# Kernel optimization log

Hardware: AMD Instinct MI355X
Metric: run time of the kernel (lower is better)

The kernel has to match this reference:

```python
import jax, jax.numpy as jnp
import numpy as np

B, V, E = 8, 12288, 98304   # batch, nodes (healpix nside=32), edges (~8 nbrs/node)
FIN, FOUT, K = 256, 256, 4  # channels, Chebyshev order
EPS = 1e-5                  # BatchNorm1d eps


def setup_inputs() -> dict:
    key = jax.random.key(0)
    ks = jax.random.split(key, 5)
    x = jax.random.normal(ks[0], (B, V, FIN), jnp.float32)
    edge_src = jax.random.randint(ks[1], (E,), 0, V, dtype=jnp.int32)
    edge_dst = jax.random.randint(ks[2], (E,), 0, V, dtype=jnp.int32)
    edge_weight = jax.random.normal(ks[3], (E,), jnp.float32) * 0.3
    scale = (2.0 / (FIN * K)) ** 0.5  # kaiming-style init over K*Fin fan-in
    weight = jax.random.normal(ks[4], (K, FIN, FOUT), jnp.float32) * scale
    bias = jnp.zeros((FOUT,), jnp.float32)
    gamma = jnp.ones((FOUT,), jnp.float32)
    beta = jnp.zeros((FOUT,), jnp.float32)
    return {"x": x, "edge_weight": edge_weight, "weight": weight, "bias": bias,
            "gamma": gamma, "beta": beta, "edge_src": edge_src, "edge_dst": edge_dst}


def reference(x, edge_weight, weight, bias, gamma, beta, edge_src, edge_dst):
    # --- ConvCheb: Chebyshev polynomial recursion over sparse Laplacian ---
    xt = x.transpose(1, 0, 2)  # [V, B, Fin] (node-major for segment scatter)

    def lmul(y):  # sparse L @ y, y: [V, B, Fin]
        msg = edge_weight[:, None, None] * y[edge_src]          # [E, B, Fin]
        return jax.ops.segment_sum(msg, edge_dst, num_segments=V)

    xs = [xt]                                  # T_0(L) x = x
    if K > 1:
        xs.append(lmul(xt))                    # T_1(L) x = L x
    for _ in range(2, K):
        xs.append(2.0 * lmul(xs[-1]) - xs[-2])  # T_k = 2 L T_{k-1} - T_{k-2}
    xk = jnp.stack(xs)                         # [K, V, B, Fin]

    out = jnp.einsum('kvbi,kio->bvo', xk, weight) + bias  # [B, V, Fout]

    # --- BatchNorm1d over channels (training-mode batch stats over B,V) ---
    mean = out.mean(axis=(0, 1))
    var = out.var(axis=(0, 1))  # biased variance, as torch uses for normalization
    out = gamma * (out - mean) * jax.lax.rsqrt(var + EPS) + beta

    return jax.nn.relu(out)
```

## Files before the change

### kernel.cpp

```cpp
#include <hip/hip_runtime.h>

#define Vn    12288
#define En    98304
#define Mrows 98304

typedef unsigned short u16;
typedef u16   u16x8  __attribute__((ext_vector_type(8)));
typedef __bf16 bf16x8 __attribute__((ext_vector_type(8)));
typedef float f32x4  __attribute__((ext_vector_type(4)));

struct __align__(8) Edge { int s; float w; };

__device__ __forceinline__ float bf2f(u16 u) {
    union { float f; unsigned int i; } c; c.i = ((unsigned int)u) << 16; return c.f;
}
__device__ __forceinline__ u16 f2bf(float f) {
    union { float f; unsigned int i; } c; c.f = f;
    unsigned int r = c.i + 0x7fffu + ((c.i >> 16) & 1u);
    return (u16)(r >> 16);
}
__device__ __forceinline__ void load_lds16(const void* g, void* l) {
    __builtin_amdgcn_global_load_lds(
        (const __attribute__((address_space(1))) void*)g,
        (__attribute__((address_space(3))) void*)l, 16, 0, 0);
}

__global__ void cvt_k(const float* __restrict__ x, u16* __restrict__ xb) {
    int v = blockIdx.x;
    int t = threadIdx.x;
    int b = t >> 5, i = (t & 31) * 8;
    const float* p = x + ((size_t)b * Vn + v) * 256 + i;
    f32x4 a0 = *(const f32x4*)p;
    f32x4 a1 = *(const f32x4*)(p + 4);
    u16x8 r;
    #pragma unroll
    for (int j = 0; j < 4; ++j) { r[j] = f2bf(a0[j]); r[4 + j] = f2bf(a1[j]); }
    *(u16x8*)(xb + (size_t)v * 2048 + b * 256 + i) = r;
}

__global__ void wtrans_k(const float* __restrict__ w, u16* __restrict__ wt) {
    int kk = blockIdx.x;
    int o  = threadIdx.x;
    wt[(size_t)o * 1024 + kk] = f2bf(w[(size_t)kk * 256 + o]);
}

__global__ void count_k(const int* __restrict__ dst, int* __restrict__ counts) {
    int e = blockIdx.x * 256 + threadIdx.x;
    atomicAdd(&counts[dst[e]], 1);
}

__global__ void scan_k(const int* __restrict__ counts, int* __restrict__ row_start,
                       int* __restrict__ cursor) {
    __shared__ int par[1024];
    int t = threadIdx.x;
    int base = t * 12;
    int s = 0;
    #pragma unroll
    for (int i = 0; i < 12; ++i) s += counts[base + i];
    par[t] = s;
    __syncthreads();
    for (int off = 1; off < 1024; off <<= 1) {
        int v_ = (t >= off) ? par[t - off] : 0;
        __syncthreads();
        par[t] += v_;
        __syncthreads();
    }
    int run = (t == 0) ? 0 : par[t - 1];
    for (int i = 0; i < 12; ++i) {
        row_start[base + i] = run;
        cursor[base + i]    = run;
        run += counts[base + i];
    }
    if (t == 1023) row_start[Vn] = En;
}

__global__ void fill_k(const int* __restrict__ src, const int* __restrict__ dst,
                       const float* __restrict__ ew, int* __restrict__ cursor,
                       Edge* __restrict__ csr) {
    int e = blockIdx.x * 256 + threadIdx.x;
    int d = dst[e];
    int p = atomicAdd(&cursor[d], 1);
    Edge ed; ed.s = src[e]; ed.w = ew[e];
    csr[p] = ed;
}

template<int PREV>
__global__ __launch_bounds__(256)
void lmul_k(const u16* __restrict__ yb, const u16* __restrict__ prevb,
            u16* __restrict__ outb, const int* __restrict__ row_start,
            const Edge* __restrict__ csr)
{
    int slice = blockIdx.x & 7;
    int v     = (blockIdx.x >> 3) * 8 + (threadIdx.x >> 5);
    int t     = threadIdx.x & 31;
    int s0    = row_start[v];
    int cnt   = row_start[v + 1] - s0;
    size_t soff = (size_t)slice * 256 + (size_t)t * 8;
    float acc[8] = {0.f,0.f,0.f,0.f,0.f,0.f,0.f,0.f};
    for (int j0 = 0; j0 < cnt; j0 += 8) {
        int ss[8]; float ww[8];
        #pragma unroll
        for (int u = 0; u < 8; ++u) {
            int j = j0 + u;
            bool ok = j < cnt;
            Edge e = csr[s0 + (ok ? j : 0)];
            ss[u] = e.s; ww[u] = ok ? e.w : 0.f;
        }
        u16x8 g[8];
        #pragma unroll
        for (int u = 0; u < 8; ++u)
            g[u] = *(const u16x8*)(yb + (size_t)ss[u] * 2048 + soff);
        #pragma unroll
        for (int u = 0; u < 8; ++u)
            #pragma unroll
            for (int j8 = 0; j8 < 8; ++j8) acc[j8] += ww[u] * bf2f(g[u][j8]);
    }
    u16x8 r;
    if (PREV) {
        u16x8 pu = *(const u16x8*)(prevb + (size_t)v * 2048 + soff);
        #pragma unroll
        for (int j8 = 0; j8 < 8; ++j8) r[j8] = f2bf(2.0f * acc[j8] - bf2f(pu[j8]));
    } else {
        #pragma unroll
        for (int j8 = 0; j8 < 8; ++j8) r[j8] = f2bf(acc[j8]);
    }
    *(u16x8*)(outb + (size_t)v * 2048 + soff) = r;
}

__device__ __forceinline__ void stage_tile(const u16* __restrict__ Ak, int k0,
                                           const u16* __restrict__ wt, int kt,
                                           int m0, int tid, int wave,
                                           char* bufA, char* bufB)
{
    #pragma unroll
    for (int r = 0; r < 2; ++r) {
        int g  = r * 512 + tid;
        int ml = g >> 3;
        int c  = (g & 7) ^ (ml & 7);
        load_lds16(Ak + ((size_t)(m0 + ml)) * 256 + k0 + c * 8,
                   bufA + r * 8192 + wave * 1024);
    }
    #pragma unroll
    for (int r = 0; r < 4; ++r) {
        int g = r * 512 + tid;
        int o = g >> 3;
        int c = (g & 7) ^ (o & 7);
        load_lds16(wt + (size_t)o * 1024 + kt * 64 + c * 8,
                   bufB + r * 8192 + wave * 1024);
    }
}

__global__ __launch_bounds__(512)
void gemm_k(const u16* __restrict__ x0, const u16* __restrict__ x1,
            const u16* __restrict__ x2, const u16* __restrict__ x3,
            const u16* __restrict__ wt, const float* __restrict__ bias,
            u16* cbp, float* __restrict__ sums, float* __restrict__ sumsq)
{
    alignas(16) __shared__ char lds[147456];
    int tid  = threadIdx.x;
    int wave = tid >> 6;
    int lane = tid & 63;
    int m0   = blockIdx.x * 128;
    int wm   = wave & 1;
    int wn   = wave >> 1;

    f32x4 acc[4][4];
    #pragma unroll
    for (int a = 0; a < 4; ++a)
        #pragma unroll
        for (int b = 0; b < 4; ++b) acc[a][b] = (f32x4){0.f,0.f,0.f,0.f};

    stage_tile(x0, 0,  wt, 0, m0, tid, wave, (char*)lds,         (char*)lds + 16384);
    stage_tile(x0, 64, wt, 1, m0, tid, wave, (char*)lds + 49152, (char*)lds + 49152 + 16384);

    int cb = 0;
    int pb = 2;
    for (int t = 0; t < 16; ++t) {
        if (t < 15) asm volatile("s_waitcnt vmcnt(6) lgkmcnt(0)" ::: "memory");
        else        asm volatile("s_waitcnt vmcnt(0) lgkmcnt(0)" ::: "memory");
        __builtin_amdgcn_s_barrier();
        __builtin_amdgcn_sched_barrier(0);
        if (t < 14) {
            int kt = t + 2;
            int ks = kt >> 2;
            int k0 = (kt & 3) * 64;
            const u16* Ak = (ks == 0) ? x0 : (ks == 1) ? x1 : (ks == 2) ? x2 : x3;
            stage_tile(Ak, k0, wt, kt, m0, tid, wave,
                       (char*)lds + pb * 49152, (char*)lds + pb * 49152 + 16384);
        }
        const char* Ab = (const char*)lds + cb * 49152;
        const char* Bb = Ab + 16384;
        #pragma unroll
        for (int kstep = 0; kstep < 2; ++kstep) {
            int cidx = kstep * 4 + (lane >> 4);
            int row  = lane & 15;
            bf16x8 af[4], bfr[4];
            #pragma unroll
            for (int mt = 0; mt < 4; ++mt) {
                int m16 = wm * 64 + mt * 16 + row;
                af[mt] = *(const bf16x8*)(Ab + (size_t)(m16 * 8 + (cidx ^ (m16 & 7))) * 16);
            }
            #pragma unroll
            for (int nt = 0; nt < 4; ++nt) {
                int ol = wn * 64 + nt * 16 + row;
                bfr[nt] = *(const bf16x8*)(Bb + (size_t)(ol * 8 + (cidx ^ (ol & 7))) * 16);
            }
            __builtin_amdgcn_s_setprio(1);
            #pragma unroll
            for (int mt = 0; mt < 4; ++mt)
                #pragma unroll
                for (int nt = 0; nt < 4; ++nt)
                    acc[mt][nt] = __builtin_amdgcn_mfma_f32_16x16x32_bf16(
                        af[mt], bfr[nt], acc[mt][nt], 0, 0, 0);
            __builtin_amdgcn_s_setprio(0);
        }
        cb = (cb == 2) ? 0 : cb + 1;
        pb = (pb == 2) ? 0 : pb + 1;
    }

    __syncthreads();
    int crow = lane & 15, quad = lane >> 4;
    #pragma unroll
    for (int nt = 0; nt < 4; ++nt) {
        int o = wn * 64 + nt * 16 + crow;
        int c_o = o >> 3, o_in = (o & 7) * 2;
        float bv = bias[o];
        float ps = 0.f, pq = 0.f;
        #pragma unroll
        for (int mt = 0; mt < 4; ++mt) {
            #pragma unroll
            for (int r = 0; r < 4; ++r) {
                int ml = wm * 64 + mt * 16 + quad * 4 + r;
                u16 q = f2bf(acc[mt][nt][r] + bv);
                float vq = bf2f(q);
                *(u16*)(lds + (size_t)ml * 512 + (size_t)(c_o ^ (ml & 7)) * 16 + o_in) = q;
                ps += vq; pq += vq * vq;
            }
        }
        ps += __shfl_down(ps, 32, 64);  pq += __shfl_down(pq, 32, 64);
        ps += __shfl_down(ps, 16, 64);  pq += __shfl_down(pq, 16, 64);
        if (quad == 0) { atomicAdd(&sums[o], ps); atomicAdd(&sumsq[o], pq); }
    }
    __syncthreads();
    #pragma unroll
    for (int rr = 0; rr < 8; ++rr) {
        int ch = rr * 512 + tid;
        int ml = ch >> 5, c = ch & 31;
        u16x8 vv = *(const u16x8*)(lds + (size_t)ml * 512 + (size_t)(c ^ (ml & 7)) * 16);
        *(u16x8*)(cbp + (size_t)(m0 + ml) * 256 + c * 8) = vv;
    }
}

__global__ void finalize_k(const float* __restrict__ sums, const float* __restrict__ sumsq,
                           const float* __restrict__ gamma, const float* __restrict__ beta,
                           float* __restrict__ scale, float* __restrict__ shift) {
    int o = threadIdx.x;
    const float invM = 1.0f / (float)Mrows;
    float mean = sums[o] * invM;
    float var  = sumsq[o] * invM - mean * mean;
    float sc   = gamma[o] * rsqrtf(var + 1e-5f);
    scale[o] = sc;
    shift[o] = beta[o] - mean * sc;
}

__global__ void bn_relu_k(const u16* __restrict__ cb, float* __restrict__ outp,
                          const float* __restrict__ scale, const float* __restrict__ shift) {
    __shared__ float ssc[256], ssh[256];
    int t = threadIdx.x;
    ssc[t] = scale[t]; ssh[t] = shift[t];
    __syncthreads();
    size_t p = ((size_t)blockIdx.x * 256 + t) * 8;
    int o0 = (int)(p & 255);
    int m  = (int)(p >> 8);
    u16x8 v = *(const u16x8*)(cb + p);
    float* dst = outp + ((size_t)((m & 7) * Vn + (m >> 3))) * 256 + o0;
    f32x4 a, c;
    #pragma unroll
    for (int i = 0; i < 4; ++i) {
        a[i] = fmaxf(bf2f(v[i])     * ssc[o0 + i]     + ssh[o0 + i],     0.f);
        c[i] = fmaxf(bf2f(v[4 + i]) * ssc[o0 + 4 + i] + ssh[o0 + 4 + i], 0.f);
    }
    __builtin_nontemporal_store(a, (f32x4*)dst);
    __builtin_nontemporal_store(c, (f32x4*)(dst + 4));
}

extern "C" void kernel_launch(void* const* d_in, const int* in_sizes, int n_in,
                              void* d_out, int out_size, void* d_ws, size_t ws_size,
                              hipStream_t stream) {
    const float* x     = (const float*)d_in[0];
    const float* ew    = (const float*)d_in[1];
    const float* w     = (const float*)d_in[2];
    const float* bias  = (const float*)d_in[3];
    const float* gamma = (const float*)d_in[4];
    const float* beta  = (const float*)d_in[5];
    const int*   esrc  = (const int*)d_in[6];
    const int*   edst  = (const int*)d_in[7];
    float* outp = (float*)d_out;
    char*  ws   = (char*)d_ws;

    u16*   xb        = (u16*)  (ws + 0);
    u16*   x1        = (u16*)  (ws + 50331648);
    u16*   x2        = (u16*)  (ws + 100663296);
    u16*   x3        = (u16*)  (ws + 150994944);
    u16*   wt        = (u16*)  (ws + 201326592);
    Edge*  csr       = (Edge*) (ws + 201850880);
    int*   counts    = (int*)  (ws + 202637312);
    int*   row_start = (int*)  (ws + 202686464);
    int*   cursor    = (int*)  (ws + 202736128);
    float* sums      = (float*)(ws + 202785280);
    float* sumsq     = (float*)(ws + 202786304);
    float* scale     = (float*)(ws + 202787328);
    float* shift     = (float*)(ws + 202788352);

    hipMemsetAsync(counts, 0, 49152, stream);
    hipMemsetAsync(sums, 0, 2048, stream);

    cvt_k<<<Vn, 256, 0, stream>>>(x, xb);
    wtrans_k<<<1024, 256, 0, stream>>>(w, wt);
    count_k<<<384, 256, 0, stream>>>(edst, counts);
    scan_k<<<1, 1024, 0, stream>>>(counts, row_start, cursor);
    fill_k<<<384, 256, 0, stream>>>(esrc, edst, ew, cursor, csr);

    lmul_k<0><<<Vn, 256, 0, stream>>>(xb, nullptr, x1, row_start, csr);
    lmul_k<1><<<Vn, 256, 0, stream>>>(x1, xb,      x2, row_start, csr);
    lmul_k<1><<<Vn, 256, 0, stream>>>(x2, x1,      x3, row_start, csr);

    gemm_k<<<Mrows / 128, 512, 0, stream>>>(xb, x1, x2, x3, wt, bias,
                                            (u16*)x1, sums, sumsq);

    finalize_k<<<1, 256, 0, stream>>>(sums, sumsq, gamma, beta, scale, shift);
    bn_relu_k<<<12288, 256, 0, stream>>>((const u16*)x1, outp, scale, shift);
}
```

Before: 467.7 us.

## Tile weight transpose via LDS, fold BN finalize into apply kernel, nontemporal loads

```diff
diff --git a/kernel.cpp b/kernel.cpp
--- a/kernel.cpp
+++ b/kernel.cpp
@@ -30,8 +30,8 @@
     int t = threadIdx.x;
     int b = t >> 5, i = (t & 31) * 8;
     const float* p = x + ((size_t)b * Vn + v) * 256 + i;
-    f32x4 a0 = *(const f32x4*)p;
-    f32x4 a1 = *(const f32x4*)(p + 4);
+    f32x4 a0 = __builtin_nontemporal_load((const f32x4*)p);
+    f32x4 a1 = __builtin_nontemporal_load((const f32x4*)(p + 4));
     u16x8 r;
     #pragma unroll
     for (int j = 0; j < 4; ++j) { r[j] = f2bf(a0[j]); r[4 + j] = f2bf(a1[j]); }
@@ -39,9 +39,22 @@
 }
 
 __global__ void wtrans_k(const float* __restrict__ w, u16* __restrict__ wt) {
-    int kk = blockIdx.x;
-    int o  = threadIdx.x;
-    wt[(size_t)o * 1024 + kk] = f2bf(w[(size_t)kk * 256 + o]);
+    __shared__ u16 tile[32][1026];
+    int o0 = blockIdx.x * 32;
+    int t  = threadIdx.x;
+    int lo = t & 31;
+    int kr = t >> 5;
+    for (int kk0 = 0; kk0 < 1024; kk0 += 8) {
+        int kk = kk0 + kr;
+        tile[lo][kk] = f2bf(w[(size_t)kk * 256 + o0 + lo]);
+    }
+    __syncthreads();
+    for (int i = 0; i < 16; ++i) {
+        int ch = i * 256 + t;
+        int r = ch >> 7, c = ch & 127;
+        u16x8 vv = *(const u16x8*)(&tile[r][c * 8]);
+        *(u16x8*)(wt + (size_t)(o0 + r) * 1024 + c * 8) = vv;
+    }
 }
 
 __global__ void count_k(const int* __restrict__ dst, int* __restrict__ counts) {
@@ -251,28 +264,24 @@
     }
 }
 
-__global__ void finalize_k(const float* __restrict__ sums, const float* __restrict__ sumsq,
-                           const float* __restrict__ gamma, const float* __restrict__ beta,
-                           float* __restrict__ scale, float* __restrict__ shift) {
-    int o = threadIdx.x;
-    const float invM = 1.0f / (float)Mrows;
-    float mean = sums[o] * invM;
-    float var  = sumsq[o] * invM - mean * mean;
-    float sc   = gamma[o] * rsqrtf(var + 1e-5f);
-    scale[o] = sc;
-    shift[o] = beta[o] - mean * sc;
-}
-
 __global__ void bn_relu_k(const u16* __restrict__ cb, float* __restrict__ outp,
-                          const float* __restrict__ scale, const float* __restrict__ shift) {
+                          const float* __restrict__ sums, const float* __restrict__ sumsq,
+                          const float* __restrict__ gamma, const float* __restrict__ beta) {
     __shared__ float ssc[256], ssh[256];
     int t = threadIdx.x;
-    ssc[t] = scale[t]; ssh[t] = shift[t];
+    {
+        const float invM = 1.0f / (float)Mrows;
+        float mean = sums[t] * invM;
+        float var  = sumsq[t] * invM - mean * mean;
+        float sc   = gamma[t] * rsqrtf(var + 1e-5f);
+        ssc[t] = sc;
+        ssh[t] = beta[t] - mean * sc;
+    }
     __syncthreads();
     size_t p = ((size_t)blockIdx.x * 256 + t) * 8;
     int o0 = (int)(p & 255);
     int m  = (int)(p >> 8);
-    u16x8 v = *(const u16x8*)(cb + p);
+    u16x8 v = __builtin_nontemporal_load((const u16x8*)(cb + p));
     float* dst = outp + ((size_t)((m & 7) * Vn + (m >> 3))) * 256 + o0;
     f32x4 a, c;
     #pragma unroll
@@ -309,14 +318,12 @@
     int*   cursor    = (int*)  (ws + 202736128);
     float* sums      = (float*)(ws + 202785280);
     float* sumsq     = (float*)(ws + 202786304);
-    float* scale     = (float*)(ws + 202787328);
-    float* shift     = (float*)(ws + 202788352);
 
     hipMemsetAsync(counts, 0, 49152, stream);
     hipMemsetAsync(sums, 0, 2048, stream);
 
     cvt_k<<<Vn, 256, 0, stream>>>(x, xb);
-    wtrans_k<<<1024, 256, 0, stream>>>(w, wt);
+    wtrans_k<<<8, 256, 0, stream>>>(w, wt);
     count_k<<<384, 256, 0, stream>>>(edst, counts);
     scan_k<<<1, 1024, 0, stream>>>(counts, row_start, cursor);
     fill_k<<<384, 256, 0, stream>>>(esrc, edst, ew, cursor, csr);
@@ -328,6 +335,5 @@
     gemm_k<<<Mrows / 128, 512, 0, stream>>>(xb, x1, x2, x3, wt, bias,
                                             (u16*)x1, sums, sumsq);
 
-    finalize_k<<<1, 256, 0, stream>>>(sums, sumsq, gamma, beta, scale, shift);
-    bn_relu_k<<<12288, 256, 0, stream>>>((const u16*)x1, outp, scale, shift);
-}
+    bn_relu_k<<<12288, 256, 0, stream>>>((const u16*)x1, outp, sums, sumsq, gamma, beta);
+}
```

Result: no change. 467.0 us (-0.1%).
